# Performance work log

Measured on AMD Instinct MI355X. Metric: run time of the kernel, lower is better.

The kernel has to match this reference:

```python
import jax, jax.numpy as jnp
import numpy as np

NUM_HEADS = 16
REF_CLUSTER = 0
TOP_RATIO = 0.3        # adaptive_sparsity(layer_idx=0) = min_sparsity
FRAME_SUBSAMPLE = 0.7  # frame_subsample_ratio in the torch code


def setup_inputs() -> dict:
    key = jax.random.key(0)
    k0, k1, k2 = jax.random.split(key, 3)
    B, S, P, C = 1, 32, 512, 1024
    N = S * P
    K, Fc = 4, 8  # K clusters of Fc frames each
    x = jax.random.normal(k0, (B, N, C), dtype=jnp.float32)
    W_qkv = jax.random.normal(k1, (C, 3 * C), dtype=jnp.float32) * (C ** -0.5)
    b_qkv = jnp.zeros((3 * C,), jnp.float32)
    W_proj = jax.random.normal(k2, (C, C), dtype=jnp.float32) * (C ** -0.5)
    b_proj = jnp.zeros((C,), jnp.float32)
    clusters = jnp.arange(S, dtype=jnp.int32).reshape(K, Fc)  # disjoint frame clusters
    keyframes = clusters[:, 0]  # one keyframe per cluster
    return {"x": x, "W_qkv": W_qkv, "b_qkv": b_qkv, "W_proj": W_proj,
            "b_proj": b_proj, "clusters": clusters, "keyframes": keyframes}


def _attn(q, k, v, scale):
    # flash_attn_func math: softmax(q k^T / sqrt(D)) v
    logits = jnp.einsum('bhqd,bhkd->bhqk', q, k) * scale
    return jnp.einsum('bhqk,bhkd->bhqd', jax.nn.softmax(logits, axis=-1), v)


def reference(x, W_qkv, b_qkv, W_proj, b_proj, clusters, keyframes):
    B, N, C = x.shape
    H = NUM_HEADS
    D = C // H
    K, Fc = clusters.shape
    S = K * Fc
    P = N // S
    scale = D ** -0.5

    # qkv projection -> q,k,v each [B, H, S, P, D]
    qkv = (x @ W_qkv + b_qkv).reshape(B, N, 3, H, D)
    q, k, v = [jnp.transpose(qkv[:, :, i], (0, 2, 1, 3)).reshape(B, H, S, P, D)
               for i in range(3)]

    # coarse: keyframe prototype scores -> topk patches per cluster
    q_proto = q[:, :, keyframes]  # [B,H,K,P,D]
    k_proto = k[:, :, keyframes]
    attn_score = jnp.mean(jnp.max(jnp.sum(k_proto * q_proto, axis=-1), axis=1), axis=0)  # [K,P]
    tk = max(1, int(P * TOP_RATIO))
    _, patch_idx = jax.lax.top_k(attn_score, tk)  # [K, tk]

    n_sub = max(1, int(Fc * FRAME_SUBSAMPLE))
    out_frames = jnp.zeros((B, H, S, P, D), x.dtype)
    for ci in range(K):
        frame_ids = clusters[ci]
        q_local = q[:, :, frame_ids].reshape(B, H, Fc * P, D)
        k_parts, v_parts = [], []
        for nc in range(K):
            # deterministic stand-in for torch.randperm frame subsampling
            sampled = clusters[nc] if nc in (REF_CLUSTER, ci) else clusters[nc][:n_sub]
            pidx = patch_idx[nc]
            k_parts.append(k[:, :, sampled][:, :, :, pidx].reshape(B, H, -1, D))
            v_parts.append(v[:, :, sampled][:, :, :, pidx].reshape(B, H, -1, D))
        k_local = jnp.concatenate(k_parts, axis=2)
        v_local = jnp.concatenate(v_parts, axis=2)
        out_local = _attn(q_local, k_local, v_local, scale).reshape(B, H, Fc, P, D)
        out_frames = out_frames.at[:, :, frame_ids].add(out_local)

    out = jnp.transpose(out_frames.reshape(B, H, N, D), (0, 2, 1, 3)).reshape(B, N, C)
    return out @ W_proj + b_proj
```

## Files before the change

kernel.cpp:

```cpp
#include <hip/hip_runtime.h>
#include <hip/hip_bf16.h>
#include <hip/hip_fp16.h>

#define DEVINL __device__ __forceinline__

using short8 = __attribute__((ext_vector_type(8))) short;
using half8  = __attribute__((ext_vector_type(8))) _Float16;
using f32x4  = __attribute__((ext_vector_type(4))) float;

static constexpr int N_TOK = 16384;
static constexpr int NH    = 16;
static constexpr int HD    = 64;
static constexpr int KCL   = 4;
static constexpr int TK    = 153;
static constexpr int LMAX  = 4096;

typedef __attribute__((address_space(1))) unsigned GU32;
typedef __attribute__((address_space(3))) unsigned LU32;

DEVINL void gload16(const void* g, void* l) {
    __builtin_amdgcn_global_load_lds((const GU32*)g, (LU32*)l, 16, 0, 0);
}

#if __has_builtin(__builtin_amdgcn_exp2f)
#define EXP2(x) __builtin_amdgcn_exp2f(x)
#else
#define EXP2(x) exp2f(x)
#endif

DEVINL unsigned short f2bf(float f) {
    unsigned u = __float_as_uint(f);
    unsigned r = u + 0x7FFFu + ((u >> 16) & 1u);
    return (unsigned short)(r >> 16);
}
DEVINL float bf2f(unsigned short h) { return __uint_as_float(((unsigned)h) << 16); }

__global__ void prep_w_kernel(const float* __restrict__ W, short* __restrict__ Btp,
                              int ncols) {
    int total = ncols * 2048;
    for (int o = blockIdx.x * blockDim.x + threadIdx.x; o < total;
         o += gridDim.x * blockDim.x) {
        int j = o >> 11, k = o & 2047, kk = k & 1023;
        float w = W[(size_t)kk * ncols + j];
        unsigned short hv = f2bf(w);
        unsigned short r = (k < 1024) ? hv : f2bf(w - bf2f(hv));
        Btp[o] = (short)r;
    }
}

template <int EPI>
__global__ __launch_bounds__(256)
void gemm_split(const float* __restrict__ xf32, const _Float16* __restrict__ xf16,
                const short* __restrict__ Btp, const float* __restrict__ bias,
                int nbn, _Float16* __restrict__ qkvh, float* __restrict__ protoF,
                float* __restrict__ outF) {
    __shared__ short Ah[4096], Al[4096], Bh[4096], Bl[4096];
    int tid = threadIdx.x, wid = tid >> 6;
    int lane = tid & 63, lr = lane & 15, lg = lane >> 4;
    int bid = blockIdx.x;
    int nb = bid % nbn, mb = bid / nbn;
    int m0 = mb * 128, n0 = nb * 128;
    int wm = wid >> 1, wn = wid & 1;

    f32x4 acc[4][4];
#pragma unroll
    for (int i = 0; i < 4; i++)
#pragma unroll
        for (int j = 0; j < 4; j++)
#pragma unroll
            for (int r = 0; r < 4; r++) acc[i][j][r] = 0.f;

    int arow = tid >> 1, ahalf = (tid & 1) * 16;
    int brow = tid >> 2, bcc = tid & 3;

    for (int kk0 = 0; kk0 < 1024; kk0 += 32) {
        gload16(Btp + (size_t)(n0 + brow) * 2048 + kk0 + bcc * 8, Bh + wid * 512);
        gload16(Btp + (size_t)(n0 + 64 + brow) * 2048 + kk0 + bcc * 8, Bh + 2048 + wid * 512);
        gload16(Btp + (size_t)(n0 + brow) * 2048 + 1024 + kk0 + bcc * 8, Bl + wid * 512);
        gload16(Btp + (size_t)(n0 + 64 + brow) * 2048 + 1024 + kk0 + bcc * 8, Bl + 2048 + wid * 512);

        float fv[16];
        if constexpr (EPI == 0) {
            const float* src = xf32 + (size_t)(m0 + arow) * 1024 + kk0 + ahalf;
#pragma unroll
            for (int q = 0; q < 4; q++) {
                f32x4 t = *(const f32x4*)(src + q * 4);
#pragma unroll
                for (int j = 0; j < 4; j++) fv[q * 4 + j] = t[j];
            }
        } else {
            const _Float16* src = xf16 + (size_t)(kk0 >> 6) * ((size_t)N_TOK * HD)
                                  + (size_t)(m0 + arow) * 64 + (kk0 & 63) + ahalf;
            half8 g0 = *(const half8*)(src), g1 = *(const half8*)(src + 8);
#pragma unroll
            for (int j = 0; j < 8; j++) { fv[j] = (float)g0[j]; fv[8 + j] = (float)g1[j]; }
        }
        short8 h8[2], l8[2];
#pragma unroll
        for (int q = 0; q < 2; q++)
#pragma unroll
            for (int j = 0; j < 8; j++) {
                float v = fv[q * 8 + j];
                unsigned short hv = f2bf(v);
                h8[q][j] = (short)hv;
                l8[q][j] = (short)f2bf(v - bf2f(hv));
            }
        *(short8*)(Ah + arow * 32 + ahalf)     = h8[0];
        *(short8*)(Ah + arow * 32 + ahalf + 8) = h8[1];
        *(short8*)(Al + arow * 32 + ahalf)     = l8[0];
        *(short8*)(Al + arow * 32 + ahalf + 8) = l8[1];
        __syncthreads();

        short8 ah[4], al[4], bh[4], bl[4];
#pragma unroll
        for (int mi = 0; mi < 4; mi++) {
            int ro = (wm * 64 + mi * 16 + lr) * 32 + lg * 8;
            ah[mi] = *(const short8*)(Ah + ro);
            al[mi] = *(const short8*)(Al + ro);
        }
#pragma unroll
        for (int ni = 0; ni < 4; ni++) {
            int ro = (wn * 64 + ni * 16 + lr) * 32 + lg * 8;
            bh[ni] = *(const short8*)(Bh + ro);
            bl[ni] = *(const short8*)(Bl + ro);
        }
#pragma unroll
        for (int mi = 0; mi < 4; mi++)
#pragma unroll
            for (int ni = 0; ni < 4; ni++) {
                acc[mi][ni] = __builtin_amdgcn_mfma_f32_16x16x32_bf16(ah[mi], bh[ni], acc[mi][ni], 0, 0, 0);
                acc[mi][ni] = __builtin_amdgcn_mfma_f32_16x16x32_bf16(al[mi], bh[ni], acc[mi][ni], 0, 0, 0);
                acc[mi][ni] = __builtin_amdgcn_mfma_f32_16x16x32_bf16(ah[mi], bl[ni], acc[mi][ni], 0, 0, 0);
            }
        __syncthreads();
    }

#pragma unroll
    for (int mi = 0; mi < 4; mi++) {
#pragma unroll
        for (int ni = 0; ni < 4; ni++) {
            int col = n0 + wn * 64 + ni * 16 + lr;
            float bv = bias[col];
#pragma unroll
            for (int r = 0; r < 4; r++) {
                int rowm = m0 + wm * 64 + mi * 16 + lg * 4 + r;
                float val = acc[mi][ni][r] + bv;
                if constexpr (EPI == 0) {
                    int i3 = col >> 10, h = (col >> 6) & 15, d = col & 63;
                    qkvh[(((size_t)i3 * NH + h) * N_TOK + rowm) * HD + d] = (_Float16)val;
                    int s = rowm >> 9;
                    if (i3 < 2 && (s & 7) == 0) {
                        int kf = s >> 3, p = rowm & 511;
                        protoF[(((size_t)i3 * KCL + kf) * 512 + p) * (NH * HD) + h * HD + d] = val;
                    }
                } else {
                    outF[(size_t)rowm * 1024 + col] = val;
                }
            }
        }
    }
}

__global__ __launch_bounds__(256)
void score_kernel(const float* __restrict__ protoF, float* __restrict__ scores) {
    int tid = threadIdx.x, lane = tid & 63;
    int pos = blockIdx.x * 4 + (tid >> 6);
    int kc = pos >> 9, p = pos & 511;
    const float* qp = protoF + ((size_t)kc * 512 + p) * (NH * HD);
    const float* kp = protoF + ((size_t)(KCL + kc) * 512 + p) * (NH * HD);
    int hh = lane >> 2, dp = (lane & 3) * 16;
    float sum = 0.f;
#pragma unroll
    for (int i = 0; i < 16; i++) sum += qp[hh * 64 + dp + i] * kp[hh * 64 + dp + i];
    sum += __shfl_xor(sum, 1, 64);
    sum += __shfl_xor(sum, 2, 64);
    float v = ((lane & 3) == 0) ? sum : -1e30f;
    for (int m = 4; m < 64; m <<= 1) v = fmaxf(v, __shfl_xor(v, m, 64));
    if (lane == 0) scores[pos] = v;
}

__global__ __launch_bounds__(64)
void topk_kernel(const float* __restrict__ scores, int* __restrict__ pidx) {
    int ci = blockIdx.x, lane = threadIdx.x;
    float v[8];
#pragma unroll
    for (int m = 0; m < 8; m++) v[m] = scores[ci * 512 + lane * 8 + m];
    for (int i = 0; i < TK; i++) {
        float best = -1e30f; int bj = 0;
#pragma unroll
        for (int m = 0; m < 8; m++) if (v[m] > best) { best = v[m]; bj = m; }
        int bidx = lane * 8 + bj;
        for (int mk = 1; mk < 64; mk <<= 1) {
            float ov = __shfl_xor(best, mk, 64);
            int   oi = __shfl_xor(bidx, mk, 64);
            if (ov > best || (ov == best && oi < bidx)) { best = ov; bidx = oi; }
        }
        bool own = ((bidx >> 3) == lane);
        int sel = bidx - lane * 8;
#pragma unroll
        for (int m = 0; m < 8; m++) if (own && m == sel) v[m] = -1e30f;
        if (lane == 0) pidx[ci * TK + i] = bidx;
    }
}

__global__ __launch_bounds__(256)
void nlist_kernel(const int* __restrict__ pidx, int* __restrict__ nlist) {
    int ci = blockIdx.x;
    int L = TK * (ci == 0 ? 23 : 26);
    for (int pos = threadIdx.x; pos < L; pos += 256) {
        int seg = pos / TK, j = pos - seg * TK;
        int nc = 0, fi = 0, acc = 0;
        for (int c = 0; c < 4; c++) {
            int cnt = (c == 0 || c == ci) ? 8 : 5;
            if (seg >= acc && seg < acc + cnt) { nc = c; fi = seg - acc; }
            acc += cnt;
        }
        nlist[ci * LMAX + pos] = (nc * 8 + fi) * 512 + pidx[nc * TK + j];
    }
}

__global__ __launch_bounds__(256)
void gatherv_kernel(const _Float16* __restrict__ qkvh, const int* __restrict__ nlist,
                    _Float16* __restrict__ vT) {
    __shared__ _Float16 vrow[64 * 80];
    int bid = blockIdx.x;
    int t64 = bid & 63, h = (bid >> 6) & 15, ci = bid >> 10;
    int L = TK * (ci == 0 ? 23 : 26);
    const _Float16* vsrc = qkvh + (size_t)2 * NH * N_TOK * HD + (size_t)h * N_TOK * HD;
    int tid = threadIdx.x;
#pragma unroll
    for (int rep = 0; rep < 2; rep++) {
        int c = rep * 256 + tid; int row = c >> 3, cc = c & 7;
        int kvg = t64 * 64 + row;
        half8 val;
#pragma unroll
        for (int j = 0; j < 8; j++) val[j] = (_Float16)0.f;
        if (kvg < L) {
            int n = nlist[ci * LMAX + kvg];
            val = *(const half8*)(vsrc + (size_t)n * HD + cc * 8);
        }
        *(half8*)(vrow + row * 80 + cc * 8) = val;
    }
    __syncthreads();
#pragma unroll
    for (int rep = 0; rep < 2; rep++) {
        int c = rep * 256 + tid; int d = c >> 3, kvc = c & 7;
        half8 ov;
#pragma unroll
        for (int j = 0; j < 8; j++) ov[j] = vrow[(kvc * 8 + j) * 80 + d];
        *(half8*)(vT + ((size_t)(ci * 16 + h) * 64 + d) * LMAX + t64 * 64 + kvc * 8) = ov;
    }
}

__global__ __launch_bounds__(512)
void attn_kernel(const _Float16* __restrict__ qkvh, const _Float16* __restrict__ vT,
                 const int* __restrict__ nlist, _Float16* __restrict__ outh) {
    __shared__ _Float16 kt[2][4096];
    __shared__ _Float16 vt[2][4096];
    __shared__ _Float16 pl[8 * 16 * 88];
    int bid = blockIdx.x;
    int qb = bid & 31, h = (bid >> 5) & 15, ci = bid >> 9;
    int tid = threadIdx.x, wid = tid >> 6, lane = tid & 63;
    int lr = lane & 15, lg = lane >> 4;
    int L = TK * (ci == 0 ? 23 : 26);
    int nt = (L + 63) >> 6;

    const _Float16* qh = qkvh;
    const _Float16* kh = qkvh + (size_t)NH * N_TOK * HD;
    int qrow0 = ci * 4096 + qb * 128 + wid * 16;

    const _Float16 qsc = (_Float16)0.180336880f;
    half8 qf[2];
#pragma unroll
    for (int ks = 0; ks < 2; ks++) {
        qf[ks] = *(const half8*)(qh + ((size_t)h * N_TOK + qrow0 + lr) * HD + ks * 32 + lg * 8);
#pragma unroll
        for (int j = 0; j < 8; j++) qf[ks][j] *= qsc;
    }
    half8 ones;
#pragma unroll
    for (int j = 0; j < 8; j++) ones[j] = (_Float16)1.f;

    f32x4 o[4], lacc;
    float mrun[4];
#pragma unroll
    for (int ni = 0; ni < 4; ni++)
#pragma unroll
        for (int r = 0; r < 4; r++) o[ni][r] = 0.f;
#pragma unroll
    for (int r = 0; r < 4; r++) { lacc[r] = 0.f; mrun[r] = -1e30f; }

    int krow = tid >> 3, kcc = tid & 7;
    int swz = (kcc ^ (krow & 7)) * 8;
    const int* nl = nlist + ci * LMAX;
    const _Float16* vTb = vT + ((size_t)(ci * 16 + h) * 64 + krow) * LMAX;
    size_t khbase = (size_t)h * N_TOK;
    _Float16* pw = pl + wid * (16 * 88);

    int n_cur = (krow < L) ? nl[krow] : 0;
    gload16(kh + (khbase + n_cur) * HD + swz, &kt[0][wid * 512]);
    gload16(vTb + swz, &vt[0][wid * 512]);
    int kvg1 = 64 + krow;
    int n_nxt = (kvg1 < L) ? nl[kvg1] : 0;

    for (int t = 0; t < nt; t++) {
        asm volatile("s_waitcnt vmcnt(0)" ::: "memory");
        __builtin_amdgcn_sched_barrier(0);
        __builtin_amdgcn_s_barrier();
        __builtin_amdgcn_sched_barrier(0);

        if (t + 1 < nt) {
            gload16(kh + (khbase + n_nxt) * HD + swz, &kt[(t + 1) & 1][wid * 512]);
            gload16(vTb + (t + 1) * 64 + swz, &vt[(t + 1) & 1][wid * 512]);
            int kvg2 = (t + 2) * 64 + krow;
            n_nxt = (kvg2 < L) ? nl[kvg2] : 0;
        }

        const _Float16* ktb = kt[t & 1];
        const _Float16* vtb = vt[t & 1];

        f32x4 s[4];
#pragma unroll
        for (int ni = 0; ni < 4; ni++) {
            f32x4 a;
#pragma unroll
            for (int r = 0; r < 4; r++) a[r] = 0.f;
#pragma unroll
            for (int ks = 0; ks < 2; ks++) {
                int row = ni * 16 + lr;
                half8 kb = *(const half8*)(ktb + row * 64 + (((ks * 4 + lg) ^ (row & 7)) * 8));
                a = __builtin_amdgcn_mfma_f32_16x16x32_f16(qf[ks], kb, a, 0, 0, 0);
            }
            s[ni] = a;
        }
        if (t == nt - 1) {
#pragma unroll
            for (int ni = 0; ni < 4; ni++) {
                int col = t * 64 + ni * 16 + lr;
                if (col >= L)
#pragma unroll
                    for (int r = 0; r < 4; r++) s[ni][r] = -1e30f;
            }
        }

        float mloc[4];
#pragma unroll
        for (int r = 0; r < 4; r++)
            mloc[r] = fmaxf(fmaxf(s[0][r], s[1][r]), fmaxf(s[2][r], s[3][r]));
        bool ok = (mloc[0] <= mrun[0] + 8.f) && (mloc[1] <= mrun[1] + 8.f) &&
                  (mloc[2] <= mrun[2] + 8.f) && (mloc[3] <= mrun[3] + 8.f);
        if (!__all(ok)) {
            float mt[4];
#pragma unroll
            for (int r = 0; r < 4; r++) mt[r] = mloc[r];
#pragma unroll
            for (int m = 1; m < 16; m <<= 1)
#pragma unroll
                for (int r = 0; r < 4; r++) mt[r] = fmaxf(mt[r], __shfl_xor(mt[r], m, 64));
#pragma unroll
            for (int r = 0; r < 4; r++) {
                float mn = fmaxf(mrun[r], mt[r]);
                float corr = EXP2(mrun[r] - mn);
                mrun[r] = mn; lacc[r] *= corr;
                o[0][r] *= corr; o[1][r] *= corr; o[2][r] *= corr; o[3][r] *= corr;
            }
        }

#pragma unroll
        for (int ni = 0; ni < 4; ni++)
#pragma unroll
            for (int r = 0; r < 4; r++)
                pw[(lg * 4 + r) * 88 + ni * 16 + lr] = (_Float16)EXP2(s[ni][r] - mrun[r]);

#pragma unroll
        for (int ks = 0; ks < 2; ks++) {
            half8 pa = *(const half8*)(pw + lr * 88 + ks * 32 + lg * 8);
#pragma unroll
            for (int ni = 0; ni < 4; ni++) {
                int vrow = ni * 16 + lr;
                half8 vb = *(const half8*)(vtb + vrow * 64 + (((ks * 4 + lg) ^ (vrow & 7)) * 8));
                o[ni] = __builtin_amdgcn_mfma_f32_16x16x32_f16(pa, vb, o[ni], 0, 0, 0);
            }
            lacc = __builtin_amdgcn_mfma_f32_16x16x32_f16(pa, ones, lacc, 0, 0, 0);
        }
    }

#pragma unroll
    for (int ni = 0; ni < 4; ni++)
#pragma unroll
        for (int r = 0; r < 4; r++) {
            float val = o[ni][r] / lacc[r];
            int qg = qrow0 + lg * 4 + r;
            outh[(size_t)h * N_TOK * HD + (size_t)qg * 64 + ni * 16 + lr] = (_Float16)val;
        }
}

extern "C" void kernel_launch(void* const* d_in, const int* in_sizes, int n_in,
                              void* d_out, int out_size, void* d_ws, size_t ws_size,
                              hipStream_t stream) {
    (void)in_sizes; (void)n_in; (void)out_size;
    const float* x     = (const float*)d_in[0];
    const float* Wqkv  = (const float*)d_in[1];
    const float* bqkv  = (const float*)d_in[2];
    const float* Wproj = (const float*)d_in[3];
    const float* bproj = (const float*)d_in[4];

    char* ws = (char*)d_ws;
    size_t off = 0;
    auto alloc = [&](size_t bytes) -> void* {
        void* p = ws + off; off += (bytes + 255) & ~(size_t)255; return p;
    };
    short*    Btp1   = (short*)alloc((size_t)3072 * 2048 * 2);
    short*    Btp2   = (short*)alloc((size_t)1024 * 2048 * 2);
    _Float16* qkvh   = (_Float16*)alloc((size_t)3 * NH * N_TOK * HD * 2);
    void*     R1     = alloc((size_t)KCL * NH * HD * LMAX * 2);
    float*    scores = (float*)alloc((size_t)KCL * 512 * 4);
    int*      pidx   = (int*)alloc((size_t)KCL * TK * 4);
    int*      nlist  = (int*)alloc((size_t)KCL * LMAX * 4);
    if (ws_size < off) return;

    float*    protoF = (float*)R1;
    _Float16* vT     = (_Float16*)R1;
    _Float16* vout   = qkvh + (size_t)2 * NH * N_TOK * HD;

    prep_w_kernel<<<2048, 256, 0, stream>>>(Wqkv, Btp1, 3072);
    prep_w_kernel<<<1024, 256, 0, stream>>>(Wproj, Btp2, 1024);

    gemm_split<0><<<128 * 24, 256, 0, stream>>>(x, nullptr, Btp1, bqkv, 24,
                                                qkvh, protoF, nullptr);

    score_kernel<<<512, 256, 0, stream>>>(protoF, scores);
    topk_kernel<<<4, 64, 0, stream>>>(scores, pidx);
    nlist_kernel<<<4, 256, 0, stream>>>(pidx, nlist);
    gatherv_kernel<<<4096, 256, 0, stream>>>(qkvh, nlist, vT);

    attn_kernel<<<2048, 512, 0, stream>>>(qkvh, vT, nlist, vout);

    gemm_split<1><<<128 * 8, 256, 0, stream>>>(nullptr, vout, Btp2, bproj, 8,
                                               nullptr, nullptr, (float*)d_out);
}
```

Measured before the change: 1.188 ms.

## Compute transposed S tiles, keep P in registers via permlane swaps, double queries per wave

The attention kernel now computes S^T (K as the A operand), so each lane holds one query's scores. P is converted to fp16 and rearranged in registers with permlane32/16 swaps, which removes the LDS round-trip for P. Each wave handles 32 query rows in two groups instead of 16, so every K/V tile loaded into LDS serves twice as many queries, and the grid is halved. The row max now needs only two cross-lane shuffles. In exchange register pressure rises and the number of blocks drops, which may lower occupancy.

```diff
diff --git a/kernel.cpp b/kernel.cpp
--- a/kernel.cpp
+++ b/kernel.cpp
@@ -6,7 +6,9 @@
 
 using short8 = __attribute__((ext_vector_type(8))) short;
 using half8  = __attribute__((ext_vector_type(8))) _Float16;
+using half2v = __attribute__((ext_vector_type(2))) _Float16;
 using f32x4  = __attribute__((ext_vector_type(4))) float;
+using uint4v = __attribute__((ext_vector_type(4))) unsigned;
 
 static constexpr int N_TOK = 16384;
 static constexpr int NH    = 16;
@@ -27,6 +29,23 @@
 #else
 #define EXP2(x) exp2f(x)
 #endif
+
+DEVINL void plswap32(unsigned& a, unsigned& b) {
+#if __has_builtin(__builtin_amdgcn_permlane32_swap)
+    auto r = __builtin_amdgcn_permlane32_swap(a, b, false, false);
+    a = r[0]; b = r[1];
+#else
+    asm volatile("v_permlane32_swap_b32 %0, %1" : "+v"(a), "+v"(b));
+#endif
+}
+DEVINL void plswap16(unsigned& a, unsigned& b) {
+#if __has_builtin(__builtin_amdgcn_permlane16_swap)
+    auto r = __builtin_amdgcn_permlane16_swap(a, b, false, false);
+    a = r[0]; b = r[1];
+#else
+    asm volatile("v_permlane16_swap_b32 %0, %1" : "+v"(a), "+v"(b));
+#endif
+}
 
 DEVINL unsigned short f2bf(float f) {
     unsigned u = __float_as_uint(f);
@@ -257,9 +276,8 @@
                  const int* __restrict__ nlist, _Float16* __restrict__ outh) {
     __shared__ _Float16 kt[2][4096];
     __shared__ _Float16 vt[2][4096];
-    __shared__ _Float16 pl[8 * 16 * 88];
     int bid = blockIdx.x;
-    int qb = bid & 31, h = (bid >> 5) & 15, ci = bid >> 9;
+    int qb = bid & 15, h = (bid >> 4) & 15, ci = bid >> 8;
     int tid = threadIdx.x, wid = tid >> 6, lane = tid & 63;
     int lr = lane & 15, lg = lane >> 4;
     int L = TK * (ci == 0 ? 23 : 26);
@@ -267,35 +285,41 @@
 
     const _Float16* qh = qkvh;
     const _Float16* kh = qkvh + (size_t)NH * N_TOK * HD;
-    int qrow0 = ci * 4096 + qb * 128 + wid * 16;
+    int qrow0 = ci * 4096 + qb * 256 + wid * 32;
 
     const _Float16 qsc = (_Float16)0.180336880f;
-    half8 qf[2];
-#pragma unroll
-    for (int ks = 0; ks < 2; ks++) {
-        qf[ks] = *(const half8*)(qh + ((size_t)h * N_TOK + qrow0 + lr) * HD + ks * 32 + lg * 8);
-#pragma unroll
-        for (int j = 0; j < 8; j++) qf[ks][j] *= qsc;
-    }
+    half8 qf[2][2];
+#pragma unroll
+    for (int g = 0; g < 2; g++)
+#pragma unroll
+        for (int ks = 0; ks < 2; ks++) {
+            qf[g][ks] = *(const half8*)(qh + ((size_t)h * N_TOK + qrow0 + g * 16 + lr) * HD
+                                        + ks * 32 + lg * 8);
+#pragma unroll
+            for (int j = 0; j < 8; j++) qf[g][ks][j] *= qsc;
+        }
     half8 ones;
 #pragma unroll
     for (int j = 0; j < 8; j++) ones[j] = (_Float16)1.f;
 
-    f32x4 o[4], lacc;
-    float mrun[4];
-#pragma unroll
-    for (int ni = 0; ni < 4; ni++)
-#pragma unroll
-        for (int r = 0; r < 4; r++) o[ni][r] = 0.f;
-#pragma unroll
-    for (int r = 0; r < 4; r++) { lacc[r] = 0.f; mrun[r] = -1e30f; }
+    f32x4 o[2][4], lacc[2];
+    float mrun[2];
+#pragma unroll
+    for (int g = 0; g < 2; g++) {
+#pragma unroll
+        for (int nd = 0; nd < 4; nd++)
+#pragma unroll
+            for (int r = 0; r < 4; r++) o[g][nd][r] = 0.f;
+#pragma unroll
+        for (int r = 0; r < 4; r++) lacc[g][r] = 0.f;
+        mrun[g] = -1e30f;
+    }
 
     int krow = tid >> 3, kcc = tid & 7;
     int swz = (kcc ^ (krow & 7)) * 8;
     const int* nl = nlist + ci * LMAX;
     const _Float16* vTb = vT + ((size_t)(ci * 16 + h) * 64 + krow) * LMAX;
     size_t khbase = (size_t)h * N_TOK;
-    _Float16* pw = pl + wid * (16 * 88);
 
     int n_cur = (krow < L) ? nl[krow] : 0;
     gload16(kh + (khbase + n_cur) * HD + swz, &kt[0][wid * 512]);
@@ -319,80 +343,116 @@
         const _Float16* ktb = kt[t & 1];
         const _Float16* vtb = vt[t & 1];
 
-        f32x4 s[4];
-#pragma unroll
-        for (int ni = 0; ni < 4; ni++) {
-            f32x4 a;
-#pragma unroll
-            for (int r = 0; r < 4; r++) a[r] = 0.f;
+        f32x4 s[2][4];
+#pragma unroll
+        for (int g = 0; g < 2; g++)
+#pragma unroll
+            for (int ni = 0; ni < 4; ni++)
+#pragma unroll
+                for (int r = 0; r < 4; r++) s[g][ni][r] = 0.f;
+#pragma unroll
+        for (int ni = 0; ni < 4; ni++)
 #pragma unroll
             for (int ks = 0; ks < 2; ks++) {
                 int row = ni * 16 + lr;
                 half8 kb = *(const half8*)(ktb + row * 64 + (((ks * 4 + lg) ^ (row & 7)) * 8));
-                a = __builtin_amdgcn_mfma_f32_16x16x32_f16(qf[ks], kb, a, 0, 0, 0);
-            }
-            s[ni] = a;
-        }
+                s[0][ni] = __builtin_amdgcn_mfma_f32_16x16x32_f16(kb, qf[0][ks], s[0][ni], 0, 0, 0);
+                s[1][ni] = __builtin_amdgcn_mfma_f32_16x16x32_f16(kb, qf[1][ks], s[1][ni], 0, 0, 0);
+            }
         if (t == nt - 1) {
 #pragma unroll
             for (int ni = 0; ni < 4; ni++) {
-                int col = t * 64 + ni * 16 + lr;
-                if (col >= L)
-#pragma unroll
-                    for (int r = 0; r < 4; r++) s[ni][r] = -1e30f;
-            }
-        }
-
-        float mloc[4];
-#pragma unroll
-        for (int r = 0; r < 4; r++)
-            mloc[r] = fmaxf(fmaxf(s[0][r], s[1][r]), fmaxf(s[2][r], s[3][r]));
-        bool ok = (mloc[0] <= mrun[0] + 8.f) && (mloc[1] <= mrun[1] + 8.f) &&
-                  (mloc[2] <= mrun[2] + 8.f) && (mloc[3] <= mrun[3] + 8.f);
+                int kvv = t * 64 + ni * 16 + lg * 4;
+#pragma unroll
+                for (int r = 0; r < 4; r++)
+                    if (kvv + r >= L) { s[0][ni][r] = -1e30f; s[1][ni][r] = -1e30f; }
+            }
+        }
+
+        float mloc[2];
+#pragma unroll
+        for (int g = 0; g < 2; g++) {
+            float m0 = fmaxf(fmaxf(s[g][0][0], s[g][0][1]), fmaxf(s[g][0][2], s[g][0][3]));
+            float m1 = fmaxf(fmaxf(s[g][1][0], s[g][1][1]), fmaxf(s[g][1][2], s[g][1][3]));
+            float m2 = fmaxf(fmaxf(s[g][2][0], s[g][2][1]), fmaxf(s[g][2][2], s[g][2][3]));
+            float m3 = fmaxf(fmaxf(s[g][3][0], s[g][3][1]), fmaxf(s[g][3][2], s[g][3][3]));
+            mloc[g] = fmaxf(fmaxf(m0, m1), fmaxf(m2, m3));
+        }
+        bool ok = (mloc[0] <= mrun[0] + 8.f) && (mloc[1] <= mrun[1] + 8.f);
         if (!__all(ok)) {
-            float mt[4];
-#pragma unroll
-            for (int r = 0; r < 4; r++) mt[r] = mloc[r];
-#pragma unroll
-            for (int m = 1; m < 16; m <<= 1)
-#pragma unroll
-                for (int r = 0; r < 4; r++) mt[r] = fmaxf(mt[r], __shfl_xor(mt[r], m, 64));
-#pragma unroll
-            for (int r = 0; r < 4; r++) {
-                float mn = fmaxf(mrun[r], mt[r]);
-                float corr = EXP2(mrun[r] - mn);
-                mrun[r] = mn; lacc[r] *= corr;
-                o[0][r] *= corr; o[1][r] *= corr; o[2][r] *= corr; o[3][r] *= corr;
-            }
-        }
-
-#pragma unroll
-        for (int ni = 0; ni < 4; ni++)
-#pragma unroll
-            for (int r = 0; r < 4; r++)
-                pw[(lg * 4 + r) * 88 + ni * 16 + lr] = (_Float16)EXP2(s[ni][r] - mrun[r]);
-
-#pragma unroll
-        for (int ks = 0; ks < 2; ks++) {
-            half8 pa = *(const half8*)(pw + lr * 88 + ks * 32 + lg * 8);
+#pragma unroll
+            for (int g = 0; g < 2; g++) {
+                float mt = mloc[g];
+                mt = fmaxf(mt, __shfl_xor(mt, 16, 64));
+                mt = fmaxf(mt, __shfl_xor(mt, 32, 64));
+                float mn = fmaxf(mrun[g], mt);
+                float corr = EXP2(mrun[g] - mn);
+                mrun[g] = mn;
+#pragma unroll
+                for (int r = 0; r < 4; r++) lacc[g][r] *= corr;
+#pragma unroll
+                for (int nd = 0; nd < 4; nd++)
+#pragma unroll
+                    for (int r = 0; r < 4; r++) o[g][nd][r] *= corr;
+            }
+        }
+
+        half8 pf[2][2];
+#pragma unroll
+        for (int g = 0; g < 2; g++) {
+            float p[4][4];
+#pragma unroll
+            for (int ni = 0; ni < 4; ni++)
+#pragma unroll
+                for (int r = 0; r < 4; r++) p[ni][r] = EXP2(s[g][ni][r] - mrun[g]);
+            unsigned c[4][2];
 #pragma unroll
             for (int ni = 0; ni < 4; ni++) {
-                int vrow = ni * 16 + lr;
-                half8 vb = *(const half8*)(vtb + vrow * 64 + (((ks * 4 + lg) ^ (vrow & 7)) * 8));
-                o[ni] = __builtin_amdgcn_mfma_f32_16x16x32_f16(pa, vb, o[ni], 0, 0, 0);
-            }
-            lacc = __builtin_amdgcn_mfma_f32_16x16x32_f16(pa, ones, lacc, 0, 0, 0);
-        }
-    }
-
-#pragma unroll
-    for (int ni = 0; ni < 4; ni++)
-#pragma unroll
-        for (int r = 0; r < 4; r++) {
-            float val = o[ni][r] / lacc[r];
-            int qg = qrow0 + lg * 4 + r;
-            outh[(size_t)h * N_TOK * HD + (size_t)qg * 64 + ni * 16 + lr] = (_Float16)val;
-        }
+                c[ni][0] = __builtin_bit_cast(unsigned, __builtin_amdgcn_cvt_pkrtz(p[ni][0], p[ni][1]));
+                c[ni][1] = __builtin_bit_cast(unsigned, __builtin_amdgcn_cvt_pkrtz(p[ni][2], p[ni][3]));
+            }
+#pragma unroll
+            for (int ksv = 0; ksv < 2; ksv++) {
+                unsigned a0 = c[2 * ksv][0], a1 = c[2 * ksv][1];
+                unsigned b0 = c[2 * ksv + 1][0], b1 = c[2 * ksv + 1][1];
+                plswap32(a0, b0); plswap32(a1, b1);
+                plswap16(a0, b0); plswap16(a1, b1);
+                uint4v w = {a0, a1, b0, b1};
+                pf[g][ksv] = __builtin_bit_cast(half8, w);
+            }
+        }
+
+#pragma unroll
+        for (int nd = 0; nd < 4; nd++)
+#pragma unroll
+            for (int ksv = 0; ksv < 2; ksv++) {
+                int row = nd * 16 + lr;
+                half8 vb = *(const half8*)(vtb + row * 64 + (((ksv * 4 + lg) ^ (row & 7)) * 8));
+                o[0][nd] = __builtin_amdgcn_mfma_f32_16x16x32_f16(vb, pf[0][ksv], o[0][nd], 0, 0, 0);
+                o[1][nd] = __builtin_amdgcn_mfma_f32_16x16x32_f16(vb, pf[1][ksv], o[1][nd], 0, 0, 0);
+            }
+#pragma unroll
+        for (int g = 0; g < 2; g++)
+#pragma unroll
+            for (int ksv = 0; ksv < 2; ksv++)
+                lacc[g] = __builtin_amdgcn_mfma_f32_16x16x32_f16(ones, pf[g][ksv], lacc[g], 0, 0, 0);
+    }
+
+#pragma unroll
+    for (int g = 0; g < 2; g++) {
+        float inv = 1.f / lacc[g][0];
+        int qg = qrow0 + g * 16 + lr;
+        unsigned* dst = (unsigned*)(outh + (size_t)h * N_TOK * HD + (size_t)qg * 64);
+#pragma unroll
+        for (int nd = 0; nd < 4; nd++)
+#pragma unroll
+            for (int rp = 0; rp < 2; rp++) {
+                half2v hv;
+                hv[0] = (_Float16)(o[g][nd][2 * rp] * inv);
+                hv[1] = (_Float16)(o[g][nd][2 * rp + 1] * inv);
+                dst[(nd * 16 + lg * 4) / 2 + rp] = __builtin_bit_cast(unsigned, hv);
+            }
+    }
 }
 
 extern "C" void kernel_launch(void* const* d_in, const int* in_sizes, int n_in,
@@ -434,7 +494,7 @@
     nlist_kernel<<<4, 256, 0, stream>>>(pidx, nlist);
     gatherv_kernel<<<4096, 256, 0, stream>>>(qkvh, nlist, vT);
 
-    attn_kernel<<<2048, 512, 0, stream>>>(qkvh, vT, nlist, vout);
+    attn_kernel<<<1024, 512, 0, stream>>>(qkvh, vT, nlist, vout);
 
     gemm_split<1><<<128 * 8, 256, 0, stream>>>(nullptr, vout, Btp2, bproj, 8,
                                                nullptr, nullptr, (float*)d_out);
```

New measurement: 1.085 ms. 1.09x faster.
